# Optimization experiments

Hardware: AMD Instinct MI355X
Metric: run time of the kernel (lower is better)

The kernel has to match this reference:

```python
import jax, jax.numpy as jnp
import numpy as np

# Sylo forward (symmetry='psd', coupling=None, bias=True, remove_diagonal=True)
# Template: T[o,c] = L[o,c] @ L[o,c]^T  (psd => R == L, no coupling)
# crosshair_dot(A,B)[i,j] = sum_k P[k,j] + sum_k P[i,k] - P[i,j], P = A*B
# crosshair_similarity sums crosshair_dot over in_channels; then +bias, zero diagonal.

N, C_IN, C_OUT, DIM, RANK = 8, 4, 64, 512, 4


def setup_inputs() -> dict:
    key = jax.random.key(0)
    kx, kl, kb = jax.random.split(key, 3)
    X = jax.random.normal(kx, (N, C_IN, DIM, DIM), dtype=jnp.float32)
    weight_L = jax.random.normal(kl, (C_OUT, C_IN, DIM, RANK), dtype=jnp.float32) * 0.05
    bias = jax.random.normal(kb, (C_OUT,), dtype=jnp.float32) * 0.05
    return {"X": X, "weight_L": weight_L, "bias": bias}


def reference(X, weight_L, bias):
    # templates: (C_out, C_in, H, W)
    T = jnp.einsum('ochr,ocwr->ochw', weight_L, weight_L)
    # P summed over in_channels: (N, C_out, H, W)
    P = jnp.einsum('nchw,ochw->nohw', X, T)
    # column sums (sum over rows h) and row sums (sum over cols w), summed over c
    col_sums = jnp.einsum('nchw,ochw->now', X, T)  # (N, C_out, W)
    row_sums = jnp.einsum('nchw,ochw->noh', X, T)  # (N, C_out, H)
    out = row_sums[..., :, None] + col_sums[..., None, :] - P
    out = out + bias[:, None, None]
    # delete diagonal
    mask = 1.0 - jnp.eye(out.shape[-1], dtype=out.dtype)
    return out * mask
```

## Files before the change

### kernel.cpp

```cpp
#include <hip/hip_runtime.h>


#define DIMS 512
#define CIN 4
#define COUT 64
#define NB 8
#define RANKS 4

typedef float f32x4 __attribute__((ext_vector_type(4)));

#define LPK_ELEMS (CIN * DIMS * COUT * RANKS)
#define SUMS_ELEMS (NB * COUT * DIMS)

__global__ __launch_bounds__(256) void pack_L(const float* __restrict__ L,
                                              float* __restrict__ Lpk) {
    int idx = blockIdx.x * 256 + threadIdx.x;
    int oc = idx & 255;
    int k  = (idx >> 8) & 511;
    int c  = idx >> 17;
    int o = oc >> 2, r = oc & 3;
    Lpk[idx] = L[((o * CIN + c) * DIMS + k) * RANKS + r];
}

#define XPAD 68

__global__ __launch_bounds__(512, 4) void sums_kernel(const float* __restrict__ X,
                                                      const float* __restrict__ Lpk,
                                                      float* __restrict__ sums) {
    const int mode = blockIdx.y;
    const int n    = blockIdx.x >> 5;
    const int d0   = (blockIdx.x & 31) << 4;
    const int t    = threadIdx.x;
    const int lane = t & 63;
    const int drow = (t >> 6) << 1;

    __shared__ float Xsm[16 * XPAD];
    const float4* __restrict__ Lpk4 = (const float4*)Lpk;

    float rsacc[2] = {0.f, 0.f};

    for (int c = 0; c < CIN; ++c) {
        float acc[2][4];
#pragma unroll
        for (int i = 0; i < 2; ++i)
#pragma unroll
            for (int j = 0; j < 4; ++j) acc[i][j] = 0.f;

        const float* __restrict__ Xc = X + (size_t)(n * CIN + c) * DIMS * DIMS;

        for (int k0 = 0; k0 < DIMS; k0 += 64) {
            __syncthreads();
            if (mode == 0) {
                int kk = t & 63, dd = t >> 6;
#pragma unroll
                for (int j = 0; j < 2; ++j)
                    Xsm[(dd + 8 * j) * XPAD + kk] = Xc[(d0 + dd + 8 * j) * DIMS + k0 + kk];
            } else {
                int dd = t & 15, kk0 = t >> 4;
#pragma unroll
                for (int j = 0; j < 2; ++j)
                    Xsm[dd * XPAD + kk0 + 32 * j] = Xc[(k0 + kk0 + 32 * j) * DIMS + d0 + dd];
            }
            __syncthreads();

#pragma unroll 2
            for (int k = 0; k < 64; k += 4) {
                float4 lv0 = Lpk4[(c * DIMS + k0 + k + 0) * 64 + lane];
                float4 lv1 = Lpk4[(c * DIMS + k0 + k + 1) * 64 + lane];
                float4 lv2 = Lpk4[(c * DIMS + k0 + k + 2) * 64 + lane];
                float4 lv3 = Lpk4[(c * DIMS + k0 + k + 3) * 64 + lane];
#pragma unroll
                for (int i = 0; i < 2; ++i) {
                    float4 xv = *(const float4*)&Xsm[(drow + i) * XPAD + k];
                    acc[i][0] += xv.x * lv0.x + xv.y * lv1.x + xv.z * lv2.x + xv.w * lv3.x;
                    acc[i][1] += xv.x * lv0.y + xv.y * lv1.y + xv.z * lv2.y + xv.w * lv3.y;
                    acc[i][2] += xv.x * lv0.z + xv.y * lv1.z + xv.z * lv2.z + xv.w * lv3.z;
                    acc[i][3] += xv.x * lv0.w + xv.y * lv1.w + xv.z * lv2.w + xv.w * lv3.w;
                }
            }
        }
#pragma unroll
        for (int i = 0; i < 2; ++i) {
            float4 lf = Lpk4[(c * DIMS + d0 + drow + i) * 64 + lane];
            rsacc[i] += lf.x * acc[i][0] + lf.y * acc[i][1] + lf.z * acc[i][2] + lf.w * acc[i][3];
        }
    }

    float* __restrict__ dst = sums + mode * SUMS_ELEMS;
#pragma unroll
    for (int i = 0; i < 2; ++i)
        dst[(n * COUT + lane) * DIMS + d0 + drow + i] = rsacc[i];
}

#define OPB 2

__global__ __launch_bounds__(256, 4) void final_kernel(const float* __restrict__ X,
                                                       const float* __restrict__ L,
                                                       const float* __restrict__ bias,
                                                       const float* __restrict__ sums,
                                                       float* __restrict__ out) {
    const int o0   = blockIdx.x * OPB;
    const int tile = blockIdx.y;
    const int h0   = (tile & 15) << 5;
    const int w0   = (tile >> 4) << 5;
    const int t    = threadIdx.x;
    const int ww4  = t & 7;
    const int hh   = t >> 3;

    __shared__ float Lhs[OPB * CIN * 32 * RANKS];
    __shared__ float Lws[OPB * CIN * 32 * RANKS];

    {
        const float4* __restrict__ L4 = (const float4*)L;
        float4* __restrict__ LhsV = (float4*)Lhs;
        float4* __restrict__ LwsV = (float4*)Lws;
        for (int idx = t; idx < 2 * OPB * CIN * 32; idx += 256) {
            int side = idx >> 8;
            int rem  = idx & 255;
            int o2   = rem >> 7;
            int c    = (rem >> 5) & 3;
            int d    = rem & 31;
            int base = side ? w0 : h0;
            float4 v = L4[((o0 + o2) * CIN + c) * DIMS + base + d];
            (side ? LwsV : LhsV)[rem] = v;
        }
    }
    __syncthreads();

    float4 Tr[OPB][CIN];
    {
        const float4* __restrict__ Lh4 = (const float4*)Lhs;
        const float4* __restrict__ Lw4 = (const float4*)Lws;
#pragma unroll
        for (int o2 = 0; o2 < OPB; ++o2)
#pragma unroll
            for (int c = 0; c < CIN; ++c) {
                float4 lh  = Lh4[(o2 * CIN + c) * 32 + hh];
                float4 wv0 = Lw4[(o2 * CIN + c) * 32 + 4 * ww4 + 0];
                float4 wv1 = Lw4[(o2 * CIN + c) * 32 + 4 * ww4 + 1];
                float4 wv2 = Lw4[(o2 * CIN + c) * 32 + 4 * ww4 + 2];
                float4 wv3 = Lw4[(o2 * CIN + c) * 32 + 4 * ww4 + 3];
                Tr[o2][c].x = lh.x * wv0.x + lh.y * wv0.y + lh.z * wv0.z + lh.w * wv0.w;
                Tr[o2][c].y = lh.x * wv1.x + lh.y * wv1.y + lh.z * wv1.z + lh.w * wv1.w;
                Tr[o2][c].z = lh.x * wv2.x + lh.y * wv2.y + lh.z * wv2.z + lh.w * wv2.w;
                Tr[o2][c].w = lh.x * wv3.x + lh.y * wv3.y + lh.z * wv3.z + lh.w * wv3.w;
            }
    }

    const float4* __restrict__ X4 = (const float4*)X;
    f32x4* __restrict__ out4      = (f32x4*)out;
    const float* __restrict__ rs  = sums;
    const float* __restrict__ cs  = sums + SUMS_ELEMS;
    const float b0 = bias[o0];
    const float b1 = bias[o0 + 1];

    const int hg  = h0 + hh;
    const int wgb = w0 + 4 * ww4;
    const size_t xoff = (size_t)hg * (DIMS / 4) + (w0 >> 2) + ww4;

    for (int n = 0; n < NB; ++n) {
        float4 p0 = {0.f, 0.f, 0.f, 0.f};
        float4 p1 = {0.f, 0.f, 0.f, 0.f};
#pragma unroll
        for (int c = 0; c < CIN; ++c) {
            float4 xv = X4[(size_t)(n * CIN + c) * (DIMS * DIMS / 4) + xoff];
            p0.x += xv.x * Tr[0][c].x;
            p0.y += xv.y * Tr[0][c].y;
            p0.z += xv.z * Tr[0][c].z;
            p0.w += xv.w * Tr[0][c].w;
            p1.x += xv.x * Tr[1][c].x;
            p1.y += xv.y * Tr[1][c].y;
            p1.z += xv.z * Tr[1][c].z;
            p1.w += xv.w * Tr[1][c].w;
        }
        {
            float  rv = rs[(n * COUT + o0) * DIMS + hg] + b0;
            float4 cv = *(const float4*)&cs[(n * COUT + o0) * DIMS + wgb];
            f32x4 ov;
            ov.x = rv + cv.x - p0.x;
            ov.y = rv + cv.y - p0.y;
            ov.z = rv + cv.z - p0.z;
            ov.w = rv + cv.w - p0.w;
            if (hg == wgb)     ov.x = 0.f;
            if (hg == wgb + 1) ov.y = 0.f;
            if (hg == wgb + 2) ov.z = 0.f;
            if (hg == wgb + 3) ov.w = 0.f;
            __builtin_nontemporal_store(ov,
                &out4[((size_t)(n * COUT + o0) * DIMS + hg) * (DIMS / 4) + (w0 >> 2) + ww4]);
        }
        {
            float  rv = rs[(n * COUT + o0 + 1) * DIMS + hg] + b1;
            float4 cv = *(const float4*)&cs[(n * COUT + o0 + 1) * DIMS + wgb];
            f32x4 ov;
            ov.x = rv + cv.x - p1.x;
            ov.y = rv + cv.y - p1.y;
            ov.z = rv + cv.z - p1.z;
            ov.w = rv + cv.w - p1.w;
            if (hg == wgb)     ov.x = 0.f;
            if (hg == wgb + 1) ov.y = 0.f;
            if (hg == wgb + 2) ov.z = 0.f;
            if (hg == wgb + 3) ov.w = 0.f;
            __builtin_nontemporal_store(ov,
                &out4[((size_t)(n * COUT + o0 + 1) * DIMS + hg) * (DIMS / 4) + (w0 >> 2) + ww4]);
        }
    }
}

extern "C" void kernel_launch(void* const* d_in, const int* in_sizes, int n_in,
                              void* d_out, int out_size, void* d_ws, size_t ws_size,
                              hipStream_t stream) {
    (void)in_sizes; (void)n_in; (void)out_size; (void)ws_size;
    const float* X    = (const float*)d_in[0];
    const float* L    = (const float*)d_in[1];
    const float* bias = (const float*)d_in[2];
    float* out = (float*)d_out;
    float* ws  = (float*)d_ws;

    float* Lpk  = ws;
    float* sums = ws + LPK_ELEMS;

    pack_L<<<LPK_ELEMS / 256, 256, 0, stream>>>(L, Lpk);
    sums_kernel<<<dim3(256, 2), 512, 0, stream>>>(X, Lpk, sums);
    final_kernel<<<dim3(COUT / OPB, 256), 256, 0, stream>>>(X, L, bias, sums, out);
}
```

Before: 824.1 us.

## Split sums kernel across channels per wave with LDS reduction; widen final kernel to 4 outputs

The sums kernel now gives each of its 4 waves one input channel and 16 rows, instead of looping over channels with 2 rows per wave. Each Lpk load is reused across 16 rows, and the per-channel partial sums are combined through shared memory at the end. The final kernel handles 4 output channels per block instead of 2, so each X load is reused across more outputs. In exchange, each thread holds more registers (16 float4 accumulators), which may lower occupancy, and the final kernel launches half as many blocks.

```diff
diff --git a/kernel.cpp b/kernel.cpp
--- a/kernel.cpp
+++ b/kernel.cpp
@@ -22,9 +22,10 @@
     Lpk[idx] = L[((o * CIN + c) * DIMS + k) * RANKS + r];
 }
 
-#define XPAD 68
-
-__global__ __launch_bounds__(512, 4) void sums_kernel(const float* __restrict__ X,
+#define XSTR 68
+#define CSTR (16 * XSTR)
+
+__global__ __launch_bounds__(256, 4) void sums_kernel(const float* __restrict__ X,
                                                       const float* __restrict__ Lpk,
                                                       float* __restrict__ sums) {
     const int mode = blockIdx.y;
@@ -32,67 +33,75 @@
     const int d0   = (blockIdx.x & 31) << 4;
     const int t    = threadIdx.x;
     const int lane = t & 63;
-    const int drow = (t >> 6) << 1;
-
-    __shared__ float Xsm[16 * XPAD];
+    const int w    = t >> 6;
+
+    __shared__ float smem[4608];
     const float4* __restrict__ Lpk4 = (const float4*)Lpk;
 
-    float rsacc[2] = {0.f, 0.f};
-
-    for (int c = 0; c < CIN; ++c) {
-        float acc[2][4];
-#pragma unroll
-        for (int i = 0; i < 2; ++i)
-#pragma unroll
-            for (int j = 0; j < 4; ++j) acc[i][j] = 0.f;
-
-        const float* __restrict__ Xc = X + (size_t)(n * CIN + c) * DIMS * DIMS;
-
-        for (int k0 = 0; k0 < DIMS; k0 += 64) {
-            __syncthreads();
-            if (mode == 0) {
-                int kk = t & 63, dd = t >> 6;
-#pragma unroll
-                for (int j = 0; j < 2; ++j)
-                    Xsm[(dd + 8 * j) * XPAD + kk] = Xc[(d0 + dd + 8 * j) * DIMS + k0 + kk];
-            } else {
-                int dd = t & 15, kk0 = t >> 4;
-#pragma unroll
-                for (int j = 0; j < 2; ++j)
-                    Xsm[dd * XPAD + kk0 + 32 * j] = Xc[(k0 + kk0 + 32 * j) * DIMS + d0 + dd];
+    float4 acc[16];
+#pragma unroll
+    for (int d = 0; d < 16; ++d) acc[d] = (float4){0.f, 0.f, 0.f, 0.f};
+
+    const float* __restrict__ Xc = X + (size_t)(n * CIN + w) * DIMS * DIMS;
+
+    for (int k0 = 0; k0 < DIMS; k0 += 64) {
+        __syncthreads();
+        if (mode == 0) {
+#pragma unroll
+            for (int j = 0; j < 16; ++j)
+                smem[w * CSTR + j * XSTR + lane] = Xc[(d0 + j) * DIMS + k0 + lane];
+        } else {
+            int dd = lane & 15, kk0 = lane >> 4;
+#pragma unroll
+            for (int j = 0; j < 16; ++j)
+                smem[w * CSTR + dd * XSTR + 4 * j + kk0] =
+                    Xc[(k0 + 4 * j + kk0) * DIMS + d0 + dd];
+        }
+        __syncthreads();
+
+#pragma unroll 2
+        for (int k = 0; k < 64; k += 4) {
+            float4 lv0 = Lpk4[(w * DIMS + k0 + k + 0) * 64 + lane];
+            float4 lv1 = Lpk4[(w * DIMS + k0 + k + 1) * 64 + lane];
+            float4 lv2 = Lpk4[(w * DIMS + k0 + k + 2) * 64 + lane];
+            float4 lv3 = Lpk4[(w * DIMS + k0 + k + 3) * 64 + lane];
+#pragma unroll
+            for (int d = 0; d < 16; ++d) {
+                float4 xv = *(const float4*)&smem[w * CSTR + d * XSTR + k];
+                acc[d].x += xv.x * lv0.x + xv.y * lv1.x + xv.z * lv2.x + xv.w * lv3.x;
+                acc[d].y += xv.x * lv0.y + xv.y * lv1.y + xv.z * lv2.y + xv.w * lv3.y;
+                acc[d].z += xv.x * lv0.z + xv.y * lv1.z + xv.z * lv2.z + xv.w * lv3.z;
+                acc[d].w += xv.x * lv0.w + xv.y * lv1.w + xv.z * lv2.w + xv.w * lv3.w;
             }
-            __syncthreads();
-
-#pragma unroll 2
-            for (int k = 0; k < 64; k += 4) {
-                float4 lv0 = Lpk4[(c * DIMS + k0 + k + 0) * 64 + lane];
-                float4 lv1 = Lpk4[(c * DIMS + k0 + k + 1) * 64 + lane];
-                float4 lv2 = Lpk4[(c * DIMS + k0 + k + 2) * 64 + lane];
-                float4 lv3 = Lpk4[(c * DIMS + k0 + k + 3) * 64 + lane];
-#pragma unroll
-                for (int i = 0; i < 2; ++i) {
-                    float4 xv = *(const float4*)&Xsm[(drow + i) * XPAD + k];
-                    acc[i][0] += xv.x * lv0.x + xv.y * lv1.x + xv.z * lv2.x + xv.w * lv3.x;
-                    acc[i][1] += xv.x * lv0.y + xv.y * lv1.y + xv.z * lv2.y + xv.w * lv3.y;
-                    acc[i][2] += xv.x * lv0.z + xv.y * lv1.z + xv.z * lv2.z + xv.w * lv3.z;
-                    acc[i][3] += xv.x * lv0.w + xv.y * lv1.w + xv.z * lv2.w + xv.w * lv3.w;
-                }
-            }
-        }
-#pragma unroll
-        for (int i = 0; i < 2; ++i) {
-            float4 lf = Lpk4[(c * DIMS + d0 + drow + i) * 64 + lane];
-            rsacc[i] += lf.x * acc[i][0] + lf.y * acc[i][1] + lf.z * acc[i][2] + lf.w * acc[i][3];
-        }
-    }
-
-    float* __restrict__ dst = sums + mode * SUMS_ELEMS;
-#pragma unroll
-    for (int i = 0; i < 2; ++i)
-        dst[(n * COUT + lane) * DIMS + d0 + drow + i] = rsacc[i];
-}
-
-#define OPB 2
+        }
+    }
+
+    float rsp[16];
+#pragma unroll
+    for (int d = 0; d < 16; ++d) {
+        float4 lf = Lpk4[(w * DIMS + d0 + d) * 64 + lane];
+        rsp[d] = lf.x * acc[d].x + lf.y * acc[d].y + lf.z * acc[d].z + lf.w * acc[d].w;
+    }
+
+    __syncthreads();
+    float* red = smem;
+#pragma unroll
+    for (int d = 0; d < 16; ++d)
+        red[(d * 4 + w) * 65 + lane] = rsp[d];
+    __syncthreads();
+
+    float* __restrict__ dst = sums + (size_t)mode * SUMS_ELEMS + (size_t)n * COUT * DIMS + d0;
+#pragma unroll
+    for (int j = 0; j < 4; ++j) {
+        int idx = 256 * j + t;
+        int d = idx & 15, o = idx >> 4;
+        float v = red[(d * 4 + 0) * 65 + o] + red[(d * 4 + 1) * 65 + o] +
+                  red[(d * 4 + 2) * 65 + o] + red[(d * 4 + 3) * 65 + o];
+        dst[o * DIMS + d] = v;
+    }
+}
+
+#define OPB 4
 
 __global__ __launch_bounds__(256, 4) void final_kernel(const float* __restrict__ X,
                                                        const float* __restrict__ L,
@@ -114,9 +123,11 @@
         const float4* __restrict__ L4 = (const float4*)L;
         float4* __restrict__ LhsV = (float4*)Lhs;
         float4* __restrict__ LwsV = (float4*)Lws;
-        for (int idx = t; idx < 2 * OPB * CIN * 32; idx += 256) {
-            int side = idx >> 8;
-            int rem  = idx & 255;
+#pragma unroll
+        for (int j = 0; j < 4; ++j) {
+            int idx  = t + 256 * j;
+            int side = idx >> 9;
+            int rem  = idx & 511;
             int o2   = rem >> 7;
             int c    = (rem >> 5) & 3;
             int d    = rem & 31;
@@ -151,57 +162,43 @@
     f32x4* __restrict__ out4      = (f32x4*)out;
     const float* __restrict__ rs  = sums;
     const float* __restrict__ cs  = sums + SUMS_ELEMS;
-    const float b0 = bias[o0];
-    const float b1 = bias[o0 + 1];
+
+    float bv[OPB];
+#pragma unroll
+    for (int o2 = 0; o2 < OPB; ++o2) bv[o2] = bias[o0 + o2];
 
     const int hg  = h0 + hh;
     const int wgb = w0 + 4 * ww4;
+    const bool z0 = (hg == wgb), z1 = (hg == wgb + 1), z2 = (hg == wgb + 2), z3 = (hg == wgb + 3);
     const size_t xoff = (size_t)hg * (DIMS / 4) + (w0 >> 2) + ww4;
 
     for (int n = 0; n < NB; ++n) {
-        float4 p0 = {0.f, 0.f, 0.f, 0.f};
-        float4 p1 = {0.f, 0.f, 0.f, 0.f};
+        float4 p[OPB];
+#pragma unroll
+        for (int o2 = 0; o2 < OPB; ++o2) p[o2] = (float4){0.f, 0.f, 0.f, 0.f};
 #pragma unroll
         for (int c = 0; c < CIN; ++c) {
             float4 xv = X4[(size_t)(n * CIN + c) * (DIMS * DIMS / 4) + xoff];
-            p0.x += xv.x * Tr[0][c].x;
-            p0.y += xv.y * Tr[0][c].y;
-            p0.z += xv.z * Tr[0][c].z;
-            p0.w += xv.w * Tr[0][c].w;
-            p1.x += xv.x * Tr[1][c].x;
-            p1.y += xv.y * Tr[1][c].y;
-            p1.z += xv.z * Tr[1][c].z;
-            p1.w += xv.w * Tr[1][c].w;
-        }
-        {
-            float  rv = rs[(n * COUT + o0) * DIMS + hg] + b0;
-            float4 cv = *(const float4*)&cs[(n * COUT + o0) * DIMS + wgb];
+#pragma unroll
+            for (int o2 = 0; o2 < OPB; ++o2) {
+                p[o2].x += xv.x * Tr[o2][c].x;
+                p[o2].y += xv.y * Tr[o2][c].y;
+                p[o2].z += xv.z * Tr[o2][c].z;
+                p[o2].w += xv.w * Tr[o2][c].w;
+            }
+        }
+#pragma unroll
+        for (int o2 = 0; o2 < OPB; ++o2) {
+            int oo = o0 + o2;
+            float  rv = rs[(n * COUT + oo) * DIMS + hg] + bv[o2];
+            float4 cv = *(const float4*)&cs[(n * COUT + oo) * DIMS + wgb];
             f32x4 ov;
-            ov.x = rv + cv.x - p0.x;
-            ov.y = rv + cv.y - p0.y;
-            ov.z = rv + cv.z - p0.z;
-            ov.w = rv + cv.w - p0.w;
-            if (hg == wgb)     ov.x = 0.f;
-            if (hg == wgb + 1) ov.y = 0.f;
-            if (hg == wgb + 2) ov.z = 0.f;
-            if (hg == wgb + 3) ov.w = 0.f;
+            ov.x = z0 ? 0.f : (rv + cv.x - p[o2].x);
+            ov.y = z1 ? 0.f : (rv + cv.y - p[o2].y);
+            ov.z = z2 ? 0.f : (rv + cv.z - p[o2].z);
+            ov.w = z3 ? 0.f : (rv + cv.w - p[o2].w);
             __builtin_nontemporal_store(ov,
-                &out4[((size_t)(n * COUT + o0) * DIMS + hg) * (DIMS / 4) + (w0 >> 2) + ww4]);
-        }
-        {
-            float  rv = rs[(n * COUT + o0 + 1) * DIMS + hg] + b1;
-            float4 cv = *(const float4*)&cs[(n * COUT + o0 + 1) * DIMS + wgb];
-            f32x4 ov;
-            ov.x = rv + cv.x - p1.x;
-            ov.y = rv + cv.y - p1.y;
-            ov.z = rv + cv.z - p1.z;
-            ov.w = rv + cv.w - p1.w;
-            if (hg == wgb)     ov.x = 0.f;
-            if (hg == wgb + 1) ov.y = 0.f;
-            if (hg == wgb + 2) ov.z = 0.f;
-            if (hg == wgb + 3) ov.w = 0.f;
-            __builtin_nontemporal_store(ov,
-                &out4[((size_t)(n * COUT + o0 + 1) * DIMS + hg) * (DIMS / 4) + (w0 >> 2) + ww4]);
+                &out4[((size_t)(n * COUT + oo) * DIMS + hg) * (DIMS / 4) + (w0 >> 2) + ww4]);
         }
     }
 }
@@ -220,6 +217,6 @@
     float* sums = ws + LPK_ELEMS;
 
     pack_L<<<LPK_ELEMS / 256, 256, 0, stream>>>(L, Lpk);
-    sums_kernel<<<dim3(256, 2), 512, 0, stream>>>(X, Lpk, sums);
+    sums_kernel<<<dim3(256, 2), 256, 0, stream>>>(X, Lpk, sums);
     final_kernel<<<dim3(COUT / OPB, 256), 256, 0, stream>>>(X, L, bias, sums, out);
 }
```

New measurement: 1.255 ms. 52.3% more time.
